# Kernel tuning notes

Hardware: AMD Instinct MI355X
Metric: run time of the kernel (lower is better)

## Reference

```python
import jax, jax.numpy as jnp
import numpy as np

V, D, F, K, L, R, ID, B = 50000, 64, 100, 3, 256, 10, 32, 128
IDMAX = 50


def _cnn(vec, Wc, bc, Wl, bl):
    # vec: [N, L, D] -> Conv1d over L (channels=D), ReLU, max-pool over L, Linear+tanh
    x = vec.transpose(0, 2, 1)  # [N, D, L]
    pad = (K - 1) // 2
    y = jax.lax.conv_general_dilated(x, Wc, (1,), [(pad, pad)],
                                     dimension_numbers=('NCH', 'OIH', 'NCH'))
    y = jax.nn.relu(y + bc[None, :, None])  # [N, F, L]
    y = y.max(axis=2)  # [N, F]
    return jnp.tanh(y @ Wl.T + bl)  # [N, ID]


def _fm(x, v, w, b):
    lin = x @ w.T + b  # [N, 1]
    i1 = x @ v
    i2 = (x ** 2) @ (v ** 2)
    pair = jnp.sum(i1 ** 2 - i2, axis=1)
    return (lin[:, 0] + 0.5 * pair)[:, None]


def setup_inputs() -> dict:
    key = jax.random.key(0)
    ks = iter(jax.random.split(key, 40))
    nrm = lambda shape, s=0.1: jax.random.normal(next(ks), shape, jnp.float32) * s
    ri = lambda shape, hi: jax.random.randint(next(ks), shape, 0, hi, dtype=jnp.int32)
    return dict(
        user_reviews=ri((B, R, L), V), item_reviews=ri((B, R, L), V),
        uids=ri((B,), IDMAX), iids=ri((B,), IDMAX),
        user2item=ri((B, R), IDMAX), item2user=ri((B, R), IDMAX),
        rand_reviews=ri((B, L), V),
        user_emb=nrm((V, D)), item_emb=nrm((V, D)),
        cu_Wc=nrm((F, D, K)), cu_bc=jnp.zeros((F,)), cu_Wl=nrm((ID, F)), cu_bl=jnp.zeros((ID,)),
        ci_Wc=nrm((F, D, K)), ci_bc=jnp.zeros((F,)), ci_Wl=nrm((ID, F)), ci_bl=jnp.zeros((ID,)),
        t_W1=nrm((ID, 2 * R * ID)), t_b1=jnp.full((ID,), 0.1),
        t_W2=nrm((ID, ID)), t_b2=jnp.full((ID,), 0.1),
        fs_v=jnp.full((ID, 8), 0.001), fs_w=nrm((1, ID), 0.001), fs_b=jnp.zeros((1,)),
        te_emb=nrm((V, D)),
        tc_Wc=nrm((F, D, K)), tc_bc=jnp.zeros((F,)), tc_Wl=nrm((ID, F)), tc_bl=jnp.zeros((ID,)),
        ft_v=jnp.full((ID, 8), 0.001), ft_w=nrm((1, ID), 0.001), ft_b=jnp.zeros((1,)),
    )


def reference(user_reviews, item_reviews, uids, iids, user2item, item2user, rand_reviews,
              user_emb, item_emb, cu_Wc, cu_bc, cu_Wl, cu_bl, ci_Wc, ci_bc, ci_Wl, ci_bl,
              t_W1, t_b1, t_W2, t_b2, fs_v, fs_w, fs_b,
              te_emb, tc_Wc, tc_bc, tc_Wl, tc_bl, ft_v, ft_w, ft_b):
    Bn = user_reviews.shape[0]
    ur = user_reviews.reshape(Bn * R, L)
    ir = item_reviews.reshape(Bn * R, L)
    # SourceNet
    ul = _cnn(user_emb[ur], cu_Wc, cu_bc, cu_Wl, cu_bl).reshape(Bn, R * ID)
    il = _cnn(item_emb[ir], ci_Wc, ci_bc, ci_Wl, ci_bl).reshape(Bn, R * ID)
    cat = jnp.concatenate([ul, il], axis=1)  # [B, 2*R*ID]
    h = jnp.tanh(cat @ t_W1.T + t_b1)
    src = jnp.tanh(h @ t_W2.T + t_b2)  # dropout in eval mode = identity
    _src_pred = _fm(jax.lax.stop_gradient(src), fs_v, fs_w, fs_b)  # computed, unused in output
    # Vectorized replacement of the per-sample membership/gather loop
    mu = user2item == iids[:, None]  # [B, R]
    mi = item2user == uids[:, None]  # [B, R]
    gu = user_reviews[jnp.arange(Bn), jnp.argmax(mu, axis=1)]  # first match
    gi = item_reviews[jnp.arange(Bn), jnp.argmax(mi, axis=1)]
    reviews = jnp.where(mu.any(1)[:, None], gu,
                        jnp.where(mi.any(1)[:, None], gi, rand_reviews))  # [B, L]
    # TargetNet
    tl = _cnn(te_emb[reviews], tc_Wc, tc_bc, tc_Wl, tc_bl)
    _tgt_pred = _fm(tl, ft_v, ft_w, ft_b)  # computed, unused in output
    return src, tl
```

## Files before the change

kernel.cpp:

```cpp
#include <hip/hip_runtime.h>
#include <hip/hip_bf16.h>


#define C_V 50000
#define C_D 64
#define C_F 100
#define C_K 3
#define C_L 256
#define C_R 10
#define C_ID 32
#define C_B 128

typedef unsigned int u32;
typedef unsigned short u16;
typedef __attribute__((ext_vector_type(8))) short bf16x8;
typedef __attribute__((ext_vector_type(4))) float f32x4;

__device__ __forceinline__ float bf2f(u16 h) { union {u32 u; float f;} v; v.u = ((u32)h) << 16; return v.f; }
__device__ __forceinline__ u16 f2bf(float f) {
    union {float f; u32 u;} v; v.f = f;
    u32 u = v.u;
    return (u16)((u + 0x7fffu + ((u >> 16) & 1u)) >> 16);
}
__device__ __forceinline__ float ldf(const void* p, int idx, int isf) {
    return isf ? ((const float*)p)[idx] : bf2f(((const u16*)p)[idx]);
}
__device__ __forceinline__ void stf(void* p, int idx, float v, int isf) {
    if (isf) ((float*)p)[idx] = v; else ((u16*)p)[idx] = f2bf(v);
}

__global__ void detect_dtype(const u32* __restrict__ ue, int* __restrict__ flag) {
    int t = threadIdx.x;
    u32 w = ue[t];
    u32 e = (w >> 7) & 0xFFu;
    int hit = (e >= 0x70u && e <= 0x7Fu);
    unsigned long long m = __ballot(hit);
    if (t == 0) flag[0] = (__popcll(m) >= 32) ? 0 : 1;
}

__global__ __launch_bounds__(256) void prep_bfrags(
    const void* __restrict__ cu_Wc, const void* __restrict__ ci_Wc,
    const void* __restrict__ tc_Wc, const int* __restrict__ flag,
    u16* __restrict__ wsB)
{
    int id = blockIdx.x * 256 + threadIdx.x;
    if (id >= 3 * 6 * 7 * 64) return;
    int isf  = flag[0];
    int s    = id / 2688;
    int rem  = id % 2688;
    int c    = rem / 448;
    int rem2 = rem % 448;
    int nt   = rem2 / 64;
    int lane = rem2 % 64;
    int f    = nt * 16 + (lane & 15);
    int quad = lane >> 4;
    const void* W = (s == 0) ? cu_Wc : (s == 1) ? ci_Wc : tc_Wc;
    u16 out[8];
    #pragma unroll
    for (int j = 0; j < 8; ++j) {
        int kdim = c * 32 + quad * 8 + j;
        int tap = kdim >> 6, d = kdim & 63;
        float v = (f < C_F) ? ldf(W, (f * C_D + d) * C_K + tap, isf) : 0.f;
        out[j] = f2bf(v);
    }
    *reinterpret_cast<uint4*>(wsB + id * 8) = *reinterpret_cast<const uint4*>(out);
}

__global__ __launch_bounds__(256) void cnn_mfma(
    const int* __restrict__ user_reviews, const int* __restrict__ item_reviews,
    const int* __restrict__ uids, const int* __restrict__ iids,
    const int* __restrict__ user2item, const int* __restrict__ item2user,
    const int* __restrict__ rand_reviews,
    const void* __restrict__ user_emb, const void* __restrict__ item_emb,
    const void* __restrict__ te_emb,
    const void* __restrict__ cu_bc, const void* __restrict__ cu_Wl, const void* __restrict__ cu_bl,
    const void* __restrict__ ci_bc, const void* __restrict__ ci_Wl, const void* __restrict__ ci_bl,
    const void* __restrict__ tc_bc, const void* __restrict__ tc_Wl, const void* __restrict__ tc_bl,
    const int* __restrict__ flag, const u16* __restrict__ wsB,
    float* __restrict__ ws_cat, void* __restrict__ d_out)
{
    __shared__ __align__(16) char smem[81760];
    u16*   embS  = (u16*)smem;
    u16*   BfS   = (u16*)(smem + 37152);
    float* poolS = (float*)(smem + 37152 + 43008);

    const int tid = threadIdx.x;
    const int idx = blockIdx.x;
    const int isf = flag[0];

    const int* toks;
    const void* emb;
    int set;
    const void *bc, *Wl, *bl;

    if (idx < C_B * C_R) {
        toks = user_reviews + idx * C_L;
        emb = user_emb; set = 0;
        bc = cu_bc; Wl = cu_Wl; bl = cu_bl;
    } else if (idx < 2 * C_B * C_R) {
        int j = idx - C_B * C_R;
        toks = item_reviews + j * C_L;
        emb = item_emb; set = 1;
        bc = ci_bc; Wl = ci_Wl; bl = ci_bl;
    } else {
        int b = idx - 2 * C_B * C_R;
        const int* t_ = rand_reviews + b * C_L;
        int iid = iids[b];
        int uid = uids[b];
        int fu = -1, fi = -1;
        for (int r = C_R - 1; r >= 0; --r) {
            if (user2item[b * C_R + r] == iid) fu = r;
            if (item2user[b * C_R + r] == uid) fi = r;
        }
        if (fu >= 0)      t_ = user_reviews + (b * C_R + fu) * C_L;
        else if (fi >= 0) t_ = item_reviews + (b * C_R + fi) * C_L;
        toks = t_;
        emb = te_emb; set = 2;
        bc = tc_bc; Wl = tc_Wl; bl = tc_bl;
    }

    {
        const uint4* src = reinterpret_cast<const uint4*>(wsB + set * 21504);
        uint4* dst = reinterpret_cast<uint4*>(BfS);
        for (int i = tid; i < 2688; i += 256) dst[i] = src[i];
    }
    if (tid < 36)            ((u32*)embS)[tid] = 0u;
    else if (tid < 72)       ((u32*)embS)[257 * 36 + (tid - 36)] = 0u;

    {
        int token = toks[tid];
        u16* dst = embS + (tid + 1) * 72;
        if (isf) {
            const float4* srow = reinterpret_cast<const float4*>(
                (const float*)emb + (size_t)token * C_D);
            #pragma unroll
            for (int j = 0; j < 8; ++j) {
                float4 a = srow[2 * j];
                float4 b = srow[2 * j + 1];
                u16 t[8] = {f2bf(a.x), f2bf(a.y), f2bf(a.z), f2bf(a.w),
                            f2bf(b.x), f2bf(b.y), f2bf(b.z), f2bf(b.w)};
                *reinterpret_cast<uint4*>(dst + j * 8) = *reinterpret_cast<const uint4*>(t);
            }
        } else {
            const uint4* srow = reinterpret_cast<const uint4*>(
                (const u16*)emb + (size_t)token * C_D);
            #pragma unroll
            for (int j = 0; j < 8; ++j)
                reinterpret_cast<uint4*>(dst)[j] = srow[j];
        }
    }
    __syncthreads();

    const int lane = tid & 63, wave = tid >> 6;
    const int quad = lane >> 4, mcol = lane & 15;
    const int mbase = wave * 64;

    f32x4 zero4 = {0.f, 0.f, 0.f, 0.f};
    f32x4 acc[4][7];
    #pragma unroll
    for (int mt = 0; mt < 4; ++mt)
        #pragma unroll
        for (int nt = 0; nt < 7; ++nt) acc[mt][nt] = zero4;

    for (int c = 0; c < 6; ++c) {
        const int tap = c >> 1, dh = c & 1;
        bf16x8 bfr[7];
        #pragma unroll
        for (int nt = 0; nt < 7; ++nt)
            bfr[nt] = *reinterpret_cast<const bf16x8*>(BfS + ((c * 7 + nt) * 64 + lane) * 8);
        bf16x8 afr[4];
        #pragma unroll
        for (int mt = 0; mt < 4; ++mt) {
            int row = mbase + mt * 16 + mcol + tap;
            afr[mt] = *reinterpret_cast<const bf16x8*>(embS + row * 72 + dh * 32 + quad * 8);
        }
        #pragma unroll
        for (int mt = 0; mt < 4; ++mt)
            #pragma unroll
            for (int nt = 0; nt < 7; ++nt)
                acc[mt][nt] = __builtin_amdgcn_mfma_f32_16x16x32_bf16(
                    afr[mt], bfr[nt], acc[mt][nt], 0, 0, 0);
    }

    #pragma unroll
    for (int nt = 0; nt < 7; ++nt) {
        float mv = -1e30f;
        #pragma unroll
        for (int mt = 0; mt < 4; ++mt) {
            mv = fmaxf(mv, fmaxf(fmaxf(acc[mt][nt].x, acc[mt][nt].y),
                                 fmaxf(acc[mt][nt].z, acc[mt][nt].w)));
        }
        mv = fmaxf(mv, __shfl_xor(mv, 16));
        mv = fmaxf(mv, __shfl_xor(mv, 32));
        int f = nt * 16 + mcol;
        if (quad == 0 && f < C_F) poolS[f * 4 + wave] = mv;
    }
    __syncthreads();

    if (tid < C_F) {
        float m4 = fmaxf(fmaxf(poolS[tid * 4 + 0], poolS[tid * 4 + 1]),
                         fmaxf(poolS[tid * 4 + 2], poolS[tid * 4 + 3]));
        poolS[tid * 4] = fmaxf(m4 + ldf(bc, tid, isf), 0.f);
    }
    __syncthreads();

    if (tid < C_ID) {
        float s = ldf(bl, tid, isf);
        for (int f = 0; f < C_F; ++f) s += poolS[f * 4] * ldf(Wl, tid * C_F + f, isf);
        float v = tanhf(s);
        if (idx < C_B * C_R) {
            int b = idx / C_R, r = idx % C_R;
            ws_cat[b * 640 + r * C_ID + tid] = v;
        } else if (idx < 2 * C_B * C_R) {
            int j = idx - C_B * C_R;
            int b = j / C_R, r = j % C_R;
            ws_cat[b * 640 + 320 + r * C_ID + tid] = v;
        } else {
            int b = idx - 2 * C_B * C_R;
            stf(d_out, C_B * C_ID + b * C_ID + tid, v, isf);
        }
    }
}

__global__ __launch_bounds__(256) void head_kernel(
    const float* __restrict__ ws_cat,
    const void* __restrict__ W1, const void* __restrict__ b1,
    const void* __restrict__ W2, const void* __restrict__ b2,
    const int* __restrict__ flag, void* __restrict__ d_out)
{
    __shared__ float part[C_ID][8];
    __shared__ float h_s[C_ID];
    int b = blockIdx.x;
    int tid = threadIdx.x;
    int isf = flag[0];
    int o = tid >> 3, seg = tid & 7;
    const float* cat = ws_cat + b * 640;
    float acc = 0.f;
    int j0 = seg * 80;
    for (int j = j0; j < j0 + 80; ++j) acc += cat[j] * ldf(W1, o * 640 + j, isf);
    part[o][seg] = acc;
    __syncthreads();
    if (tid < C_ID) {
        float s = ldf(b1, tid, isf);
        #pragma unroll
        for (int q = 0; q < 8; ++q) s += part[tid][q];
        h_s[tid] = tanhf(s);
    }
    __syncthreads();
    if (tid < C_ID) {
        float s = ldf(b2, tid, isf);
        #pragma unroll
        for (int i = 0; i < C_ID; ++i) s += h_s[i] * ldf(W2, tid * C_ID + i, isf);
        stf(d_out, b * C_ID + tid, tanhf(s), isf);
    }
}

extern "C" void kernel_launch(void* const* d_in, const int* in_sizes, int n_in,
                              void* d_out, int out_size, void* d_ws, size_t ws_size,
                              hipStream_t stream)
{
    const int* user_reviews = (const int*)d_in[0];
    const int* item_reviews = (const int*)d_in[1];
    const int* uids         = (const int*)d_in[2];
    const int* iids         = (const int*)d_in[3];
    const int* user2item    = (const int*)d_in[4];
    const int* item2user    = (const int*)d_in[5];
    const int* rand_reviews = (const int*)d_in[6];
    const void* user_emb = d_in[7];
    const void* item_emb = d_in[8];
    const void* cu_Wc = d_in[9];
    const void* cu_bc = d_in[10];
    const void* cu_Wl = d_in[11];
    const void* cu_bl = d_in[12];
    const void* ci_Wc = d_in[13];
    const void* ci_bc = d_in[14];
    const void* ci_Wl = d_in[15];
    const void* ci_bl = d_in[16];
    const void* t_W1  = d_in[17];
    const void* t_b1  = d_in[18];
    const void* t_W2  = d_in[19];
    const void* t_b2  = d_in[20];
    const void* te_emb = d_in[24];
    const void* tc_Wc  = d_in[25];
    const void* tc_bc  = d_in[26];
    const void* tc_Wl  = d_in[27];
    const void* tc_bl  = d_in[28];

    int*   ws_flag = (int*)d_ws;
    u16*   ws_B    = (u16*)((char*)d_ws + 256);
    float* ws_cat  = (float*)((char*)d_ws + 256 + 129024);

    detect_dtype<<<1, 64, 0, stream>>>((const u32*)user_emb, ws_flag);

    prep_bfrags<<<32, 256, 0, stream>>>(cu_Wc, ci_Wc, tc_Wc, ws_flag, ws_B);

    cnn_mfma<<<2 * C_B * C_R + C_B, 256, 0, stream>>>(
        user_reviews, item_reviews, uids, iids, user2item, item2user, rand_reviews,
        user_emb, item_emb, te_emb,
        cu_bc, cu_Wl, cu_bl, ci_bc, ci_Wl, ci_bl, tc_bc, tc_Wl, tc_bl,
        ws_flag, ws_B, ws_cat, d_out);

    head_kernel<<<C_B, 256, 0, stream>>>(ws_cat, t_W1, t_b1, t_W2, t_b2, ws_flag, d_out);
}
```

Measured before the change: 246.3 us.

## Read conv weight fragments from global, shrink LDS, split N-tiles, inline dtype detect

The CNN kernel no longer copies the 43 KB of conv weight fragments into shared memory. It reads them straight from global/L2 and splits the 7 N-tiles into passes of 4 and 3 to cut accumulator register pressure, with a launch bound of 3 blocks per CU. The smaller LDS footprint and fewer registers are meant to raise occupancy on the ~2700-block grid. The Linear layer after pooling is split across all 256 threads with a partial-sum reduction. The separate dtype-detect kernel is folded into each kernel, removing one launch at the cost of redundant ballots per block.

```diff
diff --git a/kernel.cpp b/kernel.cpp
--- a/kernel.cpp
+++ b/kernel.cpp
@@ -28,24 +28,23 @@
 __device__ __forceinline__ void stf(void* p, int idx, float v, int isf) {
     if (isf) ((float*)p)[idx] = v; else ((u16*)p)[idx] = f2bf(v);
 }
-
-__global__ void detect_dtype(const u32* __restrict__ ue, int* __restrict__ flag) {
-    int t = threadIdx.x;
-    u32 w = ue[t];
+__device__ __forceinline__ int detect_isf(const u32* __restrict__ ue, int lane) {
+    u32 w = ue[lane];
     u32 e = (w >> 7) & 0xFFu;
     int hit = (e >= 0x70u && e <= 0x7Fu);
     unsigned long long m = __ballot(hit);
-    if (t == 0) flag[0] = (__popcll(m) >= 32) ? 0 : 1;
+    return (__popcll(m) >= 32) ? 0 : 1;
 }
 
 __global__ __launch_bounds__(256) void prep_bfrags(
     const void* __restrict__ cu_Wc, const void* __restrict__ ci_Wc,
-    const void* __restrict__ tc_Wc, const int* __restrict__ flag,
+    const void* __restrict__ tc_Wc, const u32* __restrict__ ue,
     u16* __restrict__ wsB)
 {
-    int id = blockIdx.x * 256 + threadIdx.x;
+    int tid = threadIdx.x;
+    int isf = detect_isf(ue, tid & 63);
+    int id = blockIdx.x * 256 + tid;
     if (id >= 3 * 6 * 7 * 64) return;
-    int isf  = flag[0];
     int s    = id / 2688;
     int rem  = id % 2688;
     int c    = rem / 448;
@@ -66,7 +65,7 @@
     *reinterpret_cast<uint4*>(wsB + id * 8) = *reinterpret_cast<const uint4*>(out);
 }
 
-__global__ __launch_bounds__(256) void cnn_mfma(
+__global__ __launch_bounds__(256, 3) void cnn_mfma(
     const int* __restrict__ user_reviews, const int* __restrict__ item_reviews,
     const int* __restrict__ uids, const int* __restrict__ iids,
     const int* __restrict__ user2item, const int* __restrict__ item2user,
@@ -76,17 +75,18 @@
     const void* __restrict__ cu_bc, const void* __restrict__ cu_Wl, const void* __restrict__ cu_bl,
     const void* __restrict__ ci_bc, const void* __restrict__ ci_Wl, const void* __restrict__ ci_bl,
     const void* __restrict__ tc_bc, const void* __restrict__ tc_Wl, const void* __restrict__ tc_bl,
-    const int* __restrict__ flag, const u16* __restrict__ wsB,
+    const u16* __restrict__ wsB,
     float* __restrict__ ws_cat, void* __restrict__ d_out)
 {
-    __shared__ __align__(16) char smem[81760];
+    __shared__ __align__(16) char smem[37152 + 1600];
     u16*   embS  = (u16*)smem;
-    u16*   BfS   = (u16*)(smem + 37152);
-    float* poolS = (float*)(smem + 37152 + 43008);
+    float* poolS = (float*)(smem + 37152);
+    float* partS = (float*)smem;
 
     const int tid = threadIdx.x;
     const int idx = blockIdx.x;
-    const int isf = flag[0];
+    const int lane = tid & 63, wave = tid >> 6;
+    const int isf = detect_isf((const u32*)user_emb, lane);
 
     const int* toks;
     const void* emb;
@@ -119,11 +119,6 @@
         bc = tc_bc; Wl = tc_Wl; bl = tc_bl;
     }
 
-    {
-        const uint4* src = reinterpret_cast<const uint4*>(wsB + set * 21504);
-        uint4* dst = reinterpret_cast<uint4*>(BfS);
-        for (int i = tid; i < 2688; i += 256) dst[i] = src[i];
-    }
     if (tid < 36)            ((u32*)embS)[tid] = 0u;
     else if (tid < 72)       ((u32*)embS)[257 * 36 + (tid - 36)] = 0u;
 
@@ -151,49 +146,86 @@
     }
     __syncthreads();
 
-    const int lane = tid & 63, wave = tid >> 6;
     const int quad = lane >> 4, mcol = lane & 15;
     const int mbase = wave * 64;
-
-    f32x4 zero4 = {0.f, 0.f, 0.f, 0.f};
-    f32x4 acc[4][7];
-    #pragma unroll
-    for (int mt = 0; mt < 4; ++mt)
-        #pragma unroll
-        for (int nt = 0; nt < 7; ++nt) acc[mt][nt] = zero4;
-
-    for (int c = 0; c < 6; ++c) {
-        const int tap = c >> 1, dh = c & 1;
-        bf16x8 bfr[7];
-        #pragma unroll
-        for (int nt = 0; nt < 7; ++nt)
-            bfr[nt] = *reinterpret_cast<const bf16x8*>(BfS + ((c * 7 + nt) * 64 + lane) * 8);
-        bf16x8 afr[4];
-        #pragma unroll
-        for (int mt = 0; mt < 4; ++mt) {
-            int row = mbase + mt * 16 + mcol + tap;
-            afr[mt] = *reinterpret_cast<const bf16x8*>(embS + row * 72 + dh * 32 + quad * 8);
-        }
+    const u16* BfG = wsB + set * 21504;
+
+    {
+        f32x4 acc[4][4];
         #pragma unroll
         for (int mt = 0; mt < 4; ++mt)
             #pragma unroll
-            for (int nt = 0; nt < 7; ++nt)
-                acc[mt][nt] = __builtin_amdgcn_mfma_f32_16x16x32_bf16(
-                    afr[mt], bfr[nt], acc[mt][nt], 0, 0, 0);
-    }
-
-    #pragma unroll
-    for (int nt = 0; nt < 7; ++nt) {
-        float mv = -1e30f;
-        #pragma unroll
-        for (int mt = 0; mt < 4; ++mt) {
-            mv = fmaxf(mv, fmaxf(fmaxf(acc[mt][nt].x, acc[mt][nt].y),
-                                 fmaxf(acc[mt][nt].z, acc[mt][nt].w)));
-        }
-        mv = fmaxf(mv, __shfl_xor(mv, 16));
-        mv = fmaxf(mv, __shfl_xor(mv, 32));
-        int f = nt * 16 + mcol;
-        if (quad == 0 && f < C_F) poolS[f * 4 + wave] = mv;
+            for (int nt = 0; nt < 4; ++nt) acc[mt][nt] = (f32x4){0.f,0.f,0.f,0.f};
+        #pragma unroll
+        for (int c = 0; c < 6; ++c) {
+            const int tap = c >> 1, dh = c & 1;
+            bf16x8 bfr[4];
+            #pragma unroll
+            for (int nt = 0; nt < 4; ++nt)
+                bfr[nt] = *reinterpret_cast<const bf16x8*>(BfG + ((c * 7 + nt) * 64 + lane) * 8);
+            bf16x8 afr[4];
+            #pragma unroll
+            for (int mt = 0; mt < 4; ++mt) {
+                int row = mbase + mt * 16 + mcol + tap;
+                afr[mt] = *reinterpret_cast<const bf16x8*>(embS + row * 72 + dh * 32 + quad * 8);
+            }
+            #pragma unroll
+            for (int mt = 0; mt < 4; ++mt)
+                #pragma unroll
+                for (int nt = 0; nt < 4; ++nt)
+                    acc[mt][nt] = __builtin_amdgcn_mfma_f32_16x16x32_bf16(
+                        afr[mt], bfr[nt], acc[mt][nt], 0, 0, 0);
+        }
+        #pragma unroll
+        for (int nt = 0; nt < 4; ++nt) {
+            float mv = -1e30f;
+            #pragma unroll
+            for (int mt = 0; mt < 4; ++mt)
+                mv = fmaxf(mv, fmaxf(fmaxf(acc[mt][nt].x, acc[mt][nt].y),
+                                     fmaxf(acc[mt][nt].z, acc[mt][nt].w)));
+            mv = fmaxf(mv, __shfl_xor(mv, 16));
+            mv = fmaxf(mv, __shfl_xor(mv, 32));
+            if (quad == 0) poolS[(nt * 16 + mcol) * 4 + wave] = mv;
+        }
+    }
+    {
+        f32x4 acc[4][3];
+        #pragma unroll
+        for (int mt = 0; mt < 4; ++mt)
+            #pragma unroll
+            for (int nt = 0; nt < 3; ++nt) acc[mt][nt] = (f32x4){0.f,0.f,0.f,0.f};
+        #pragma unroll
+        for (int c = 0; c < 6; ++c) {
+            const int tap = c >> 1, dh = c & 1;
+            bf16x8 bfr[3];
+            #pragma unroll
+            for (int nt = 0; nt < 3; ++nt)
+                bfr[nt] = *reinterpret_cast<const bf16x8*>(BfG + ((c * 7 + 4 + nt) * 64 + lane) * 8);
+            bf16x8 afr[4];
+            #pragma unroll
+            for (int mt = 0; mt < 4; ++mt) {
+                int row = mbase + mt * 16 + mcol + tap;
+                afr[mt] = *reinterpret_cast<const bf16x8*>(embS + row * 72 + dh * 32 + quad * 8);
+            }
+            #pragma unroll
+            for (int mt = 0; mt < 4; ++mt)
+                #pragma unroll
+                for (int nt = 0; nt < 3; ++nt)
+                    acc[mt][nt] = __builtin_amdgcn_mfma_f32_16x16x32_bf16(
+                        afr[mt], bfr[nt], acc[mt][nt], 0, 0, 0);
+        }
+        #pragma unroll
+        for (int nt = 0; nt < 3; ++nt) {
+            float mv = -1e30f;
+            #pragma unroll
+            for (int mt = 0; mt < 4; ++mt)
+                mv = fmaxf(mv, fmaxf(fmaxf(acc[mt][nt].x, acc[mt][nt].y),
+                                     fmaxf(acc[mt][nt].z, acc[mt][nt].w)));
+            mv = fmaxf(mv, __shfl_xor(mv, 16));
+            mv = fmaxf(mv, __shfl_xor(mv, 32));
+            int f = (4 + nt) * 16 + mcol;
+            if (quad == 0 && f < C_F) poolS[f * 4 + wave] = mv;
+        }
     }
     __syncthreads();
 
@@ -204,9 +236,22 @@
     }
     __syncthreads();
 
+    {
+        int o = tid >> 3, seg = tid & 7;
+        int f0 = (seg < 4) ? seg * 13 : 52 + (seg - 4) * 12;
+        int cnt = (seg < 4) ? 13 : 12;
+        float acc = 0.f;
+        for (int q = 0; q < cnt; ++q) {
+            int f = f0 + q;
+            acc += poolS[f * 4] * ldf(Wl, o * C_F + f, isf);
+        }
+        partS[o * 8 + seg] = acc;
+    }
+    __syncthreads();
     if (tid < C_ID) {
         float s = ldf(bl, tid, isf);
-        for (int f = 0; f < C_F; ++f) s += poolS[f * 4] * ldf(Wl, tid * C_F + f, isf);
+        #pragma unroll
+        for (int q = 0; q < 8; ++q) s += partS[tid * 8 + q];
         float v = tanhf(s);
         if (idx < C_B * C_R) {
             int b = idx / C_R, r = idx % C_R;
@@ -226,13 +271,13 @@
     const float* __restrict__ ws_cat,
     const void* __restrict__ W1, const void* __restrict__ b1,
     const void* __restrict__ W2, const void* __restrict__ b2,
-    const int* __restrict__ flag, void* __restrict__ d_out)
+    const u32* __restrict__ ue, void* __restrict__ d_out)
 {
     __shared__ float part[C_ID][8];
     __shared__ float h_s[C_ID];
     int b = blockIdx.x;
     int tid = threadIdx.x;
-    int isf = flag[0];
+    int isf = detect_isf(ue, tid & 63);
     int o = tid >> 3, seg = tid & 7;
     const float* cat = ws_cat + b * 640;
     float acc = 0.f;
@@ -286,19 +331,18 @@
     const void* tc_Wl  = d_in[27];
     const void* tc_bl  = d_in[28];
 
-    int*   ws_flag = (int*)d_ws;
-    u16*   ws_B    = (u16*)((char*)d_ws + 256);
-    float* ws_cat  = (float*)((char*)d_ws + 256 + 129024);
-
-    detect_dtype<<<1, 64, 0, stream>>>((const u32*)user_emb, ws_flag);
-
-    prep_bfrags<<<32, 256, 0, stream>>>(cu_Wc, ci_Wc, tc_Wc, ws_flag, ws_B);
+    u16*   ws_B   = (u16*)d_ws;
+    float* ws_cat = (float*)((char*)d_ws + 129536);
+
+    prep_bfrags<<<32, 256, 0, stream>>>(cu_Wc, ci_Wc, tc_Wc,
+                                        (const u32*)user_emb, ws_B);
 
     cnn_mfma<<<2 * C_B * C_R + C_B, 256, 0, stream>>>(
         user_reviews, item_reviews, uids, iids, user2item, item2user, rand_reviews,
         user_emb, item_emb, te_emb,
         cu_bc, cu_Wl, cu_bl, ci_bc, ci_Wl, ci_bl, tc_bc, tc_Wl, tc_bl,
-        ws_flag, ws_B, ws_cat, d_out);
-
-    head_kernel<<<C_B, 256, 0, stream>>>(ws_cat, t_W1, t_b1, t_W2, t_b2, ws_flag, d_out);
-}
+        ws_B, ws_cat, d_out);
+
+    head_kernel<<<C_B, 256, 0, stream>>>(ws_cat, t_W1, t_b1, t_W2, t_b2,
+                                         (const u32*)user_emb, d_out);
+}
```

After: 210.7 us. 14.4% less time.
